# Optimization experiments

Measured on AMD Instinct MI355X. Metric: run time of the kernel, lower is better.

Reference implementation:

```python
import jax, jax.numpy as jnp
import numpy as np
import math

B, P, N, D = 64, 96, 12, 2048
W = P - N + 1  # 85 sliding windows
SCALE = 1.0 / math.sqrt(2048.0)
LN_EPS = 1e-5


def setup_inputs() -> dict:
    key = jax.random.key(0)
    ks = jax.random.split(key, 16)
    g = lambda k, shape: (jax.random.normal(k, shape, dtype=jnp.float32) * 0.02)
    return {
        "fc_feats": jax.random.normal(ks[0], (B, P, D), dtype=jnp.float32),
        "nsa_q_w": g(ks[1], (D, D)), "nsa_q_b": jnp.zeros((D,), jnp.float32),
        "nsa_k_w": g(ks[2], (D, D)), "nsa_k_b": jnp.zeros((D,), jnp.float32),
        "nsa_v_w": g(ks[3], (D, D)), "nsa_v_b": jnp.zeros((D,), jnp.float32),
        "nsa_fc_w": g(ks[4], (N, N)), "nsa_fc_b": jnp.zeros((N,), jnp.float32),
        "ds_w": g(ks[5], (W, P)), "ds_b": jnp.zeros((W,), jnp.float32),
        "ln_g": jnp.ones((D,), jnp.float32), "ln_b": jnp.zeros((D,), jnp.float32),
        "sa_q_w": g(ks[6], (D, D)), "sa_q_b": jnp.zeros((D,), jnp.float32),
        "sa_k_w": g(ks[7], (D, D)), "sa_k_b": jnp.zeros((D,), jnp.float32),
        "sa_v_w": g(ks[8], (D, D)), "sa_v_b": jnp.zeros((D,), jnp.float32),
        "sa_fc_w": g(ks[9], (W, W)), "sa_fc_b": jnp.zeros((W,), jnp.float32),
    }


def _encoder(fc_feats, nsa_q_w, nsa_q_b, nsa_k_w, nsa_k_b, nsa_v_w, nsa_v_b,
             nsa_fc_w, nsa_fc_b, ds_w, ds_b, ln_g, ln_b,
             sa_q_w, sa_q_b, sa_k_w, sa_k_b, sa_v_w, sa_v_b, sa_fc_w, sa_fc_b):
    # ---- Neighboring self-attention over all W sliding windows at once ----
    idx = jnp.arange(W)[:, None] + jnp.arange(N)[None, :]      # [W, N]
    win = fc_feats[:, idx, :]                                  # [B, W, N, D]
    q = jnp.einsum('bwnd,ed->bwne', win, nsa_q_w) + nsa_q_b
    k = jnp.einsum('bwnd,ed->bwne', win, nsa_k_w) + nsa_k_b
    v = jnp.einsum('bwnd,ed->bwne', win, nsa_v_w) + nsa_v_b
    attn = jax.nn.softmax(jnp.einsum('bwne,bwme->bwnm', q, k) * SCALE, axis=-1)
    nf = jnp.einsum('bwnm,bwmd->bwnd', attn, v)                # [B, W, N, D]
    # mask is a constant ones buffer [B,1,N] fed through fc + softmax
    mask = jnp.ones((B, N), jnp.float32)
    wmask = jax.nn.softmax(mask @ nsa_fc_w.T + nsa_fc_b, axis=-1)  # [B, N]
    nsa_feats = jnp.einsum('bn,bwnd->bwd', wmask, nf)          # [B, W, D]

    # ---- downsample over the image axis: Linear(P -> W) ----
    new_fc = jnp.einsum('bpd,wp->bwd', fc_feats, ds_w) + ds_b[None, :, None]

    # ---- residual + LayerNorm over D ----
    x = new_fc + nsa_feats
    mu = jnp.mean(x, axis=-1, keepdims=True)
    var = jnp.mean(jnp.square(x - mu), axis=-1, keepdims=True)
    x = (x - mu) * jax.lax.rsqrt(var + LN_EPS) * ln_g + ln_b   # [B, W, D]

    # ---- global self-attention over the W positions ----
    q2 = jnp.einsum('bwd,ed->bwe', x, sa_q_w) + sa_q_b
    k2 = jnp.einsum('bwd,ed->bwe', x, sa_k_w) + sa_k_b
    v2 = jnp.einsum('bwd,ed->bwe', x, sa_v_w) + sa_v_b
    attn2 = jax.nn.softmax(jnp.einsum('bwe,bue->bwu', q2, k2) * SCALE, axis=-1)
    nf2 = jnp.einsum('bwu,bud->bwd', attn2, v2)                # [B, W, D]
    mask2 = jnp.ones((B, W), jnp.float32)
    wmask2 = jax.nn.softmax(mask2 @ sa_fc_w.T + sa_fc_b, axis=-1)  # [B, W]
    return jnp.einsum('bw,bwd->bd', wmask2, nf2)               # [B, D]


def reference(fc_feats, nsa_q_w, nsa_q_b, nsa_k_w, nsa_k_b, nsa_v_w, nsa_v_b,
              nsa_fc_w, nsa_fc_b, ds_w, ds_b, ln_g, ln_b,
              sa_q_w, sa_q_b, sa_k_w, sa_k_b, sa_v_w, sa_v_b, sa_fc_w, sa_fc_b):
    return _encoder(fc_feats, nsa_q_w, nsa_q_b, nsa_k_w, nsa_k_b, nsa_v_w, nsa_v_b,
                    nsa_fc_w, nsa_fc_b, ds_w, ds_b, ln_g, ln_b,
                    sa_q_w, sa_q_b, sa_k_w, sa_k_b, sa_v_w, sa_v_b, sa_fc_w, sa_fc_b)
```

## Files before the change

kernel.cpp:

```cpp
#include <hip/hip_runtime.h>
#include <hip/hip_bf16.h>

#define DEV __device__ __forceinline__

typedef __attribute__((ext_vector_type(8))) short s16x8;
typedef __attribute__((ext_vector_type(4))) float f32x4;

#define B_ 64
#define P_ 96
#define N_ 12
#define D_ 2048
#define W_ 85
#define M1_ (B_ * P_)
#define M2_ (B_ * W_)
#define M2P_ 5504
#define SCALE_F 0.02209708691207961f
#define LN_EPS_F 1e-5f

DEV float b2f(short h) { return __uint_as_float(((unsigned)(unsigned short)h) << 16); }
DEV short f2b(float f) {
  __hip_bfloat16 h = __float2bfloat16(f);
  return *reinterpret_cast<short*>(&h);
}

DEV void gload_lds16(const void* g, void* l) {
  __builtin_amdgcn_global_load_lds(
      (const __attribute__((address_space(1))) unsigned int*)(unsigned long long)g,
      (__attribute__((address_space(3))) unsigned int*)(unsigned int)(unsigned long long)l,
      16, 0, 0);
}

__global__ __launch_bounds__(256) void castA_kernel(const float* s, short* d, int n) {
  const int i = (blockIdx.x * 256 + threadIdx.x) * 8;
  if (i >= n) return;
  float4 a = *(const float4*)(s + i);
  float4 b = *(const float4*)(s + i + 4);
  s16x8 o;
  o[0] = f2b(a.x); o[1] = f2b(a.y); o[2] = f2b(a.z); o[3] = f2b(a.w);
  o[4] = f2b(b.x); o[5] = f2b(b.y); o[6] = f2b(b.z); o[7] = f2b(b.w);
  *(s16x8*)(d + i) = o;
}

struct Cast2 { const float* s[2]; short* d[2]; };

__global__ __launch_bounds__(256) void cast2_kernel(Cast2 j, int n) {
  const int jb = blockIdx.y;
  const int i = (blockIdx.x * 256 + threadIdx.x) * 8;
  if (i >= n) return;
  const float* src = j.s[jb] + i;
  float4 a = *(const float4*)(src);
  float4 b = *(const float4*)(src + 4);
  s16x8 o;
  o[0] = f2b(a.x); o[1] = f2b(a.y); o[2] = f2b(a.z); o[3] = f2b(a.w);
  o[4] = f2b(b.x); o[5] = f2b(b.y); o[6] = f2b(b.z); o[7] = f2b(b.w);
  *(s16x8*)(j.d[jb] + i) = o;
}

struct Cast4T { const float* s[4]; short* d[4]; };

__global__ __launch_bounds__(256) void castT_kernel(Cast4T j) {
  __shared__ float tl[64][65];
  const int z = blockIdx.z;
  const float* src = j.s[z];
  short* dst = j.d[z];
  const int e0 = blockIdx.x * 64, d0 = blockIdx.y * 64;
  const int t = threadIdx.x;
  for (int i = t; i < 64 * 16; i += 256) {
    const int er = i >> 4, c4 = (i & 15) * 4;
    const float4 v = *(const float4*)(src + (long)(e0 + er) * 2048 + d0 + c4);
    tl[c4 + 0][er] = v.x;
    tl[c4 + 1][er] = v.y;
    tl[c4 + 2][er] = v.z;
    tl[c4 + 3][er] = v.w;
  }
  __syncthreads();
  for (int i = t; i < 64 * 8; i += 256) {
    const int dr = i >> 3, e8 = (i & 7) * 8;
    s16x8 o;
#pragma unroll
    for (int e = 0; e < 8; ++e) o[e] = f2b(tl[dr][e8 + e]);
    *(s16x8*)(dst + (long)(d0 + dr) * 2048 + e0 + e8) = o;
  }
}

__global__ __launch_bounds__(256) void prep_kernel(const float* nw, const float* nb,
                                                   const float* sw, const float* sb, float* wm,
                                                   const float* wk1, const float* bq1, float* r1,
                                                   const float* wk2, const float* bq2, float* r2) {
  const int bx = blockIdx.x, t = threadIdx.x;
  if (bx == 0) {
    __shared__ float l1[12], l2[85];
    if (t < 12) { float s = nb[t]; for (int n = 0; n < 12; ++n) s += nw[t * 12 + n]; l1[t] = s; }
    if (t < 85) { float s = sb[t]; for (int w = 0; w < 85; ++w) s += sw[t * 85 + w]; l2[t] = s; }
    __syncthreads();
    if (t == 0) {
      float m = l1[0]; for (int i = 1; i < 12; ++i) m = fmaxf(m, l1[i]);
      float s = 0.f; float e[12];
      for (int i = 0; i < 12; ++i) { e[i] = expf(l1[i] - m); s += e[i]; }
      for (int i = 0; i < 12; ++i) wm[i] = e[i] / s;
    } else if (t == 64) {
      float m = l2[0]; for (int i = 1; i < 85; ++i) m = fmaxf(m, l2[i]);
      float s = 0.f;
      for (int i = 0; i < 85; ++i) s += expf(l2[i] - m);
      for (int i = 0; i < 85; ++i) wm[16 + i] = expf(l2[i] - m) / s;
    }
    return;
  }
  const int idx = bx - 1;
  const int stage = idx >> 6;
  const int ec = (idx & 63) >> 3, dpc = idx & 7;
  const float* wk = stage ? wk2 : wk1;
  const float* bq = stage ? bq2 : bq1;
  float* r = stage ? r2 : r1;
  const int dp = dpc * 256 + t;
  const int e0 = ec * 256;
  float s = 0.f;
  for (int e = e0; e < e0 + 256; ++e) s += bq[e] * wk[(long)e * 2048 + dp];
  atomicAdd(&r[dp], s);
}

struct GemmArgs {
  const short* A[3];
  const short* Wt[3];
  const float* bias[3];
  void* C[3];
  int mlim;
};

template <int OM>
__global__ __launch_bounds__(256) void gemm_nt_bf16(GemmArgs g) {
  __shared__ short As[4096];
  __shared__ short Bs[4096];
  const int z = blockIdx.z;
  const short* A = g.A[z];
  const short* Wm = g.Wt[z];
  const int tid = threadIdx.x, wave = tid >> 6, lane = tid & 63;
  const int wmo = (wave >> 1) * 64, wno = (wave & 1) * 64;
  const long rowA0 = (long)blockIdx.x * 128;
  const long rowB0 = (long)blockIdx.y * 128;
  const int kg = lane >> 4, rsub = lane & 15;

  f32x4 acc[4][4];
  const f32x4 zz = {0.f, 0.f, 0.f, 0.f};
#pragma unroll
  for (int i = 0; i < 4; ++i)
#pragma unroll
    for (int jj = 0; jj < 4; ++jj) acc[i][jj] = zz;

  for (int kt = 0; kt < 64; ++kt) {
    const int kbase = kt * 32;
    __syncthreads();
#pragma unroll
    for (int i = 0; i < 2; ++i) {
      const int row = i * 64 + lane;
      gload_lds16(A + (rowA0 + row) * 2048 + kbase + wave * 8,
                  (char*)As + (wave * 128 + i * 64) * 16);
      gload_lds16(Wm + (rowB0 + row) * 2048 + kbase + wave * 8,
                  (char*)Bs + (wave * 128 + i * 64) * 16);
    }
    __syncthreads();
    s16x8 af[4], bv[4];
#pragma unroll
    for (int f = 0; f < 4; ++f) {
      af[f] = *(const s16x8*)(As + (kg * 128 + wmo + f * 16 + rsub) * 8);
      bv[f] = *(const s16x8*)(Bs + (kg * 128 + wno + f * 16 + rsub) * 8);
    }
#pragma unroll
    for (int i = 0; i < 4; ++i)
#pragma unroll
      for (int jj = 0; jj < 4; ++jj)
        acc[i][jj] = __builtin_amdgcn_mfma_f32_16x16x32_bf16(af[i], bv[jj], acc[i][jj], 0, 0, 0);
  }

  const float* bias = g.bias[z];
#pragma unroll
  for (int i = 0; i < 4; ++i) {
    const long row = rowA0 + wmo + i * 16 + (lane >> 4) * 4;
#pragma unroll
    for (int jj = 0; jj < 4; ++jj) {
      const long col = rowB0 + wno + jj * 16 + (lane & 15);
      const float bvl = bias ? bias[col] : 0.f;
#pragma unroll
      for (int r = 0; r < 4; ++r) {
        if (row + r < g.mlim) {
          if (OM == 0)
            ((short*)g.C[z])[(row + r) * 2048 + col] = f2b(acc[i][jj][r] + bvl);
          else
            ((float*)g.C[z])[(row + r) * 2048 + col] = acc[i][jj][r] + bvl;
        }
      }
    }
  }
}

template <int STAGE>
__global__ __launch_bounds__(256) void attn_mfma_kernel(const short* Aq, const short* Bk,
                                                        const float* wm, float* outp) {
  __shared__ short As[8][96][8];
  __shared__ short Bs[8][96][8];
  __shared__ float S[96][97];
  __shared__ float C1[85][12];
  __shared__ float M1[85][12];
  const int b = blockIdx.x;
  const int tid = threadIdx.x, wave = tid >> 6, lane = tid & 63;
  const int RPB = (STAGE == 1) ? 96 : 85;
  const long base = (long)b * RPB * 2048;
  const int wr0 = (wave >> 1) * 48, wc0 = (wave & 1) * 48;
  const int fr = lane & 15, fk = lane >> 4;

  f32x4 acc[3][3];
  const f32x4 zz = {0.f, 0.f, 0.f, 0.f};
#pragma unroll
  for (int i = 0; i < 3; ++i)
#pragma unroll
    for (int j = 0; j < 3; ++j) acc[i][j] = zz;

  for (int kt = 0; kt < 32; ++kt) {
    const int kb = kt * 64;
    __syncthreads();
#pragma unroll
    for (int it = 0; it < 3; ++it) {
      const int u = it * 256 + tid;
      const int row = u % 96, kg = u / 96;
      gload_lds16(Aq + base + (long)row * 2048 + kb + kg * 8, (char*)As + u * 16);
      gload_lds16(Bk + base + (long)row * 2048 + kb + kg * 8, (char*)Bs + u * 16);
    }
    __syncthreads();
#pragma unroll
    for (int ks = 0; ks < 2; ++ks) {
      const int kgx = ks * 4 + fk;
      s16x8 af[3], bv[3];
#pragma unroll
      for (int i = 0; i < 3; ++i) {
        af[i] = *(const s16x8*)&As[kgx][wr0 + i * 16 + fr][0];
        bv[i] = *(const s16x8*)&Bs[kgx][wc0 + i * 16 + fr][0];
      }
#pragma unroll
      for (int i = 0; i < 3; ++i)
#pragma unroll
        for (int j = 0; j < 3; ++j)
          acc[i][j] = __builtin_amdgcn_mfma_f32_16x16x32_bf16(af[i], bv[j], acc[i][j], 0, 0, 0);
    }
  }
#pragma unroll
  for (int i = 0; i < 3; ++i)
#pragma unroll
    for (int j = 0; j < 3; ++j)
#pragma unroll
      for (int r = 0; r < 4; ++r)
        S[wr0 + i * 16 + fk * 4 + r][wc0 + j * 16 + fr] = acc[i][j][r];
  __syncthreads();

  if (STAGE == 2) {
    if (tid < 85) {
      float mx = -1e30f;
      for (int u = 0; u < 85; ++u) mx = fmaxf(mx, S[tid][u]);
      float sum = 0.f;
      for (int u = 0; u < 85; ++u) {
        const float e = expf((S[tid][u] - mx) * SCALE_F);
        S[tid][u] = e;
        sum += e;
      }
      (&C1[0][0])[tid] = wm[tid] / sum;
    }
    __syncthreads();
    if (tid < 85) {
      float a = 0.f;
      for (int i = 0; i < 85; ++i) a += (&C1[0][0])[i] * S[i][tid];
      outp[b * 85 + tid] = a;
    }
  } else {
    for (int p = tid; p < 85 * 12; p += 256) {
      const int w = p / 12, n = p % 12;
      const int row = w + n;
      float mx = -1e30f;
      for (int m = 0; m < 12; ++m) mx = fmaxf(mx, S[row][w + m]);
      float sum = 0.f;
      for (int m = 0; m < 12; ++m) sum += expf((S[row][w + m] - mx) * SCALE_F);
      M1[w][n] = mx;
      C1[w][n] = wm[n] / sum;
    }
    __syncthreads();
    for (int p = tid; p < 85 * 12; p += 256) {
      const int w = p / 12, m = p % 12;
      float a = 0.f;
#pragma unroll
      for (int n = 0; n < 12; ++n)
        a += C1[w][n] * expf((S[w + n][w + m] - M1[w][n]) * SCALE_F);
      outp[(b * 85 + w) * 12 + m] = a;
    }
  }
}

__global__ __launch_bounds__(256) void combine_kernel(const float* fc32, const short* vp,
                                                      const float* p1, const float* dsw_g,
                                                      const float* dsb, float* X) {
  const int b = blockIdx.y, d0 = blockIdx.x * 128;
  const int t = threadIdx.x;
  __shared__ float fcs[96][128];
  __shared__ short vps[96][128];
  __shared__ float dsw[85][96];
  __shared__ float p1s[85][12];
  for (int s = t; s < 96 * 32; s += 256) {
    const int row = s >> 5, c4 = (s & 31) * 4;
    *(float4*)&fcs[row][c4] = *(const float4*)(fc32 + ((long)b * 96 + row) * 2048 + d0 + c4);
  }
  for (int s = t; s < 96 * 16; s += 256) {
    const int row = s >> 4, c8 = (s & 15) * 8;
    *(s16x8*)&vps[row][c8] = *(const s16x8*)(vp + ((long)b * 96 + row) * 2048 + d0 + c8);
  }
  for (int s = t; s < 85 * 96; s += 256) (&dsw[0][0])[s] = dsw_g[s];
  for (int s = t; s < 85 * 12; s += 256) (&p1s[0][0])[s] = p1[(long)b * 85 * 12 + s];
  __syncthreads();
  const int dp = (t & 63) * 2, wslot = t >> 6;
  for (int w = wslot; w < 85; w += 4) {
    float a0 = dsb[w], a1 = a0;
    for (int p = 0; p < 96; ++p) {
      const float c = dsw[w][p];
      a0 += c * fcs[p][dp];
      a1 += c * fcs[p][dp + 1];
    }
#pragma unroll
    for (int m = 0; m < 12; ++m) {
      const unsigned vv = *(const unsigned*)&vps[w + m][dp];
      const float c = p1s[w][m];
      a0 += c * __uint_as_float(vv << 16);
      a1 += c * __uint_as_float(vv & 0xffff0000u);
    }
    const long o = ((long)b * 85 + w) * 2048 + d0 + dp;
    X[o] = a0;
    X[o + 1] = a1;
  }
}

__global__ __launch_bounds__(256) void ln_kernel(const float* X, const float* gam,
                                                 const float* bet, short* XLN) {
  const long row = blockIdx.x;
  const int t = threadIdx.x;
  float v[8];
  *(float4*)&v[0] = *(const float4*)(X + row * 2048 + t * 8);
  *(float4*)&v[4] = *(const float4*)(X + row * 2048 + t * 8 + 4);
  float s = 0.f, q = 0.f;
#pragma unroll
  for (int e = 0; e < 8; ++e) { s += v[e]; q += v[e] * v[e]; }
#pragma unroll
  for (int o = 32; o > 0; o >>= 1) { s += __shfl_down(s, o); q += __shfl_down(q, o); }
  __shared__ float rs[4], rq[4];
  if ((t & 63) == 0) { rs[t >> 6] = s; rq[t >> 6] = q; }
  __syncthreads();
  const float S = rs[0] + rs[1] + rs[2] + rs[3];
  const float Q = rq[0] + rq[1] + rq[2] + rq[3];
  const float mu = S * (1.f / 2048.f);
  const float var = Q * (1.f / 2048.f) - mu * mu;
  const float rstd = rsqrtf(var + LN_EPS_F);
  s16x8 o8;
#pragma unroll
  for (int e = 0; e < 8; ++e) {
    const int c = t * 8 + e;
    o8[e] = f2b((v[e] - mu) * rstd * gam[c] + bet[c]);
  }
  *(s16x8*)(XLN + row * 2048 + t * 8) = o8;
}

__global__ __launch_bounds__(256) void z2_kernel(const short* xln, const float* p2, short* z2) {
  const int b = blockIdx.y, d = blockIdx.x * 256 + threadIdx.x;
  if (b >= 64) { z2[(long)b * 2048 + d] = 0; return; }
  __shared__ float pc[85];
  if (threadIdx.x < 85) pc[threadIdx.x] = p2[b * 85 + threadIdx.x];
  __syncthreads();
  float a = 0.f;
  for (int u = 0; u < 85; ++u) a += pc[u] * b2f(xln[((long)b * 85 + u) * 2048 + d]);
  z2[(long)b * 2048 + d] = f2b(a);
}

extern "C" void kernel_launch(void* const* d_in, const int* in_sizes, int n_in,
                              void* d_out, int out_size, void* d_ws, size_t ws_size,
                              hipStream_t stream) {
  char* ws = (char*)d_ws;
  size_t off = 0;
  auto alloc = [&](size_t bytes) -> char* {
    char* p = ws + off;
    off += (bytes + 255) & ~(size_t)255;
    return p;
  };

  short* A1   = (short*)alloc((size_t)M1_ * D_ * 2);
  short* WqT1 = (short*)alloc((size_t)D_ * D_ * 2);
  short* WkT1 = (short*)alloc((size_t)D_ * D_ * 2);
  short* WqT2 = (short*)alloc((size_t)D_ * D_ * 2);
  short* WkT2 = (short*)alloc((size_t)D_ * D_ * 2);
  short* Gt1  = (short*)alloc((size_t)D_ * D_ * 2);
  short* Gt2  = (short*)alloc((size_t)D_ * D_ * 2);
  short* Wv1c = (short*)alloc((size_t)D_ * D_ * 2);
  short* Wv2c = (short*)alloc((size_t)D_ * D_ * 2);
  short* Y1   = (short*)alloc((size_t)M1_ * D_ * 2);
  short* VP   = (short*)alloc((size_t)M1_ * D_ * 2);
  float* X    = (float*)alloc((size_t)M2_ * D_ * 4);
  float* P1   = (float*)alloc((size_t)B_ * W_ * N_ * 4);
  short* Z2   = (short*)alloc((size_t)128 * D_ * 2);
  float* P2   = (float*)alloc((size_t)B_ * W_ * 4);
  float* WM   = (float*)alloc(512);
  float* R1   = (float*)alloc(D_ * 4);
  float* R2   = (float*)alloc(D_ * 4);

  short* XLN = A1;
  short* Y2  = Y1;

  if (off > ws_size) return;

  const size_t zbytes = (size_t)((char*)R2 - (char*)P2) + D_ * 4;
  hipMemsetAsync(P2, 0, zbytes, stream);

  castA_kernel<<<dim3(6144), 256, 0, stream>>>((const float*)d_in[0], A1, M1_ * D_);
  Cast4T ct;
  ct.s[0] = (const float*)d_in[1];  ct.d[0] = WqT1;
  ct.s[1] = (const float*)d_in[3];  ct.d[1] = WkT1;
  ct.s[2] = (const float*)d_in[13]; ct.d[2] = WqT2;
  ct.s[3] = (const float*)d_in[15]; ct.d[3] = WkT2;
  castT_kernel<<<dim3(32, 32, 4), 256, 0, stream>>>(ct);
  Cast2 cv;
  cv.s[0] = (const float*)d_in[5];  cv.d[0] = Wv1c;
  cv.s[1] = (const float*)d_in[17]; cv.d[1] = Wv2c;
  cast2_kernel<<<dim3(2048, 2), 256, 0, stream>>>(cv, D_ * D_);
  prep_kernel<<<dim3(129), 256, 0, stream>>>(
      (const float*)d_in[7], (const float*)d_in[8],
      (const float*)d_in[19], (const float*)d_in[20], WM,
      (const float*)d_in[3], (const float*)d_in[2], R1,
      (const float*)d_in[15], (const float*)d_in[14], R2);

  GemmArgs gg;
  gg.A[0] = WkT1; gg.Wt[0] = WqT1; gg.bias[0] = nullptr; gg.C[0] = Gt1;
  gg.A[1] = WkT2; gg.Wt[1] = WqT2; gg.bias[1] = nullptr; gg.C[1] = Gt2;
  gg.mlim = 2048;
  gemm_nt_bf16<0><<<dim3(16, 16, 2), 256, 0, stream>>>(gg);

  GemmArgs g1;
  g1.A[0] = A1; g1.Wt[0] = Wv1c; g1.bias[0] = (const float*)d_in[6]; g1.C[0] = VP;
  g1.A[1] = A1; g1.Wt[1] = Gt1;  g1.bias[1] = R1;                    g1.C[1] = Y1;
  g1.mlim = M1_;
  gemm_nt_bf16<0><<<dim3(48, 16, 2), 256, 0, stream>>>(g1);

  attn_mfma_kernel<1><<<dim3(64), 256, 0, stream>>>(Y1, A1, WM, P1);

  combine_kernel<<<dim3(16, 64), 256, 0, stream>>>((const float*)d_in[0], VP, P1,
                                                   (const float*)d_in[9],
                                                   (const float*)d_in[10], X);
  ln_kernel<<<dim3(5440), 256, 0, stream>>>(X, (const float*)d_in[11], (const float*)d_in[12], XLN);

  GemmArgs g2;
  g2.A[0] = XLN; g2.Wt[0] = Gt2; g2.bias[0] = R2; g2.C[0] = Y2;
  g2.mlim = M2P_;
  gemm_nt_bf16<0><<<dim3(43, 16, 1), 256, 0, stream>>>(g2);

  attn_mfma_kernel<2><<<dim3(64), 256, 0, stream>>>(Y2, XLN, WM + 16, P2);

  z2_kernel<<<dim3(8, 128), 256, 0, stream>>>(XLN, P2, Z2);

  GemmArgs go;
  go.A[0] = Z2; go.Wt[0] = Wv2c; go.bias[0] = (const float*)d_in[18]; go.C[0] = d_out;
  go.mlim = 64;
  gemm_nt_bf16<1><<<dim3(1, 16, 1), 256, 0, stream>>>(go);
}
```

Before: 889.9 us.

## Double-buffer LDS tiles in GEMM/attention and split-K the output GEMM

Adds LDS double buffering to the main bf16 GEMM and the attention score kernels, so the global-to-LDS load of the next K tile overlaps the MFMA work on the current one and one barrier per iteration is dropped. Replaces the single-block-row output GEMM (16 blocks) with a dedicated split-K kernel using 64 blocks that accumulates into the output with atomics, after a memset of the output. It also shrinks the Z2 padding from 128 to 64 rows. The cost is doubled LDS use, which may lower occupancy, plus float atomics and their nondeterministic summation order.

```diff
diff --git a/kernel.cpp b/kernel.cpp
--- a/kernel.cpp
+++ b/kernel.cpp
@@ -129,8 +129,8 @@
 
 template <int OM>
 __global__ __launch_bounds__(256) void gemm_nt_bf16(GemmArgs g) {
-  __shared__ short As[4096];
-  __shared__ short Bs[4096];
+  __shared__ short As[2][4096];
+  __shared__ short Bs[2][4096];
   const int z = blockIdx.z;
   const short* A = g.A[z];
   const short* Wm = g.Wt[z];
@@ -147,29 +147,34 @@
 #pragma unroll
     for (int jj = 0; jj < 4; ++jj) acc[i][jj] = zz;
 
-  for (int kt = 0; kt < 64; ++kt) {
-    const int kbase = kt * 32;
-    __syncthreads();
+  auto stage = [&](int bb, int kbase) {
 #pragma unroll
     for (int i = 0; i < 2; ++i) {
       const int row = i * 64 + lane;
       gload_lds16(A + (rowA0 + row) * 2048 + kbase + wave * 8,
-                  (char*)As + (wave * 128 + i * 64) * 16);
+                  (char*)As[bb] + (wave * 128 + i * 64) * 16);
       gload_lds16(Wm + (rowB0 + row) * 2048 + kbase + wave * 8,
-                  (char*)Bs + (wave * 128 + i * 64) * 16);
-    }
-    __syncthreads();
+                  (char*)Bs[bb] + (wave * 128 + i * 64) * 16);
+    }
+  };
+
+  stage(0, 0);
+  __syncthreads();
+  for (int kt = 0; kt < 64; ++kt) {
+    const int cur = kt & 1;
+    if (kt < 63) stage(cur ^ 1, (kt + 1) * 32);
     s16x8 af[4], bv[4];
 #pragma unroll
     for (int f = 0; f < 4; ++f) {
-      af[f] = *(const s16x8*)(As + (kg * 128 + wmo + f * 16 + rsub) * 8);
-      bv[f] = *(const s16x8*)(Bs + (kg * 128 + wno + f * 16 + rsub) * 8);
+      af[f] = *(const s16x8*)(As[cur] + (kg * 128 + wmo + f * 16 + rsub) * 8);
+      bv[f] = *(const s16x8*)(Bs[cur] + (kg * 128 + wno + f * 16 + rsub) * 8);
     }
 #pragma unroll
     for (int i = 0; i < 4; ++i)
 #pragma unroll
       for (int jj = 0; jj < 4; ++jj)
         acc[i][jj] = __builtin_amdgcn_mfma_f32_16x16x32_bf16(af[i], bv[jj], acc[i][jj], 0, 0, 0);
+    __syncthreads();
   }
 
   const float* bias = g.bias[z];
@@ -193,11 +198,69 @@
   }
 }
 
+__global__ __launch_bounds__(256) void out_gemm_kernel(const short* A, const short* Wm,
+                                                       const float* bias, float* C) {
+  __shared__ short As[2][4][64][8];
+  __shared__ short Bs[2][4][128][8];
+  const int kz = blockIdx.x;
+  const long rowB0 = (long)blockIdx.y * 128;
+  const int tid = threadIdx.x, wave = tid >> 6, lane = tid & 63;
+  const int wno = wave * 32;
+  const int kgx = lane >> 4, rsub = lane & 15;
+
+  f32x4 acc[4][2];
+  const f32x4 zz = {0.f, 0.f, 0.f, 0.f};
+#pragma unroll
+  for (int f = 0; f < 4; ++f) { acc[f][0] = zz; acc[f][1] = zz; }
+
+  auto stage = [&](int bb, int kbase) {
+    gload_lds16(A + (long)lane * 2048 + kbase + wave * 8, (char*)As[bb] + tid * 16);
+#pragma unroll
+    for (int i = 0; i < 2; ++i) {
+      const int row = i * 64 + lane;
+      gload_lds16(Wm + (rowB0 + row) * 2048 + kbase + wave * 8,
+                  (char*)Bs[bb] + (wave * 128 + i * 64) * 16);
+    }
+  };
+
+  const int kb0 = kz * 512;
+  stage(0, kb0);
+  __syncthreads();
+  for (int kt = 0; kt < 16; ++kt) {
+    const int cur = kt & 1;
+    if (kt < 15) stage(cur ^ 1, kb0 + (kt + 1) * 32);
+    s16x8 af[4], bv[2];
+#pragma unroll
+    for (int f = 0; f < 4; ++f) af[f] = *(const s16x8*)&As[cur][kgx][f * 16 + rsub][0];
+#pragma unroll
+    for (int j = 0; j < 2; ++j) bv[j] = *(const s16x8*)&Bs[cur][kgx][wno + j * 16 + rsub][0];
+#pragma unroll
+    for (int f = 0; f < 4; ++f)
+#pragma unroll
+      for (int j = 0; j < 2; ++j)
+        acc[f][j] = __builtin_amdgcn_mfma_f32_16x16x32_bf16(af[f], bv[j], acc[f][j], 0, 0, 0);
+    __syncthreads();
+  }
+
+#pragma unroll
+  for (int f = 0; f < 4; ++f) {
+    const int row = f * 16 + (lane >> 4) * 4;
+#pragma unroll
+    for (int j = 0; j < 2; ++j) {
+      const long col = rowB0 + wno + j * 16 + (lane & 15);
+      const float bvl = (kz == 0) ? bias[col] : 0.f;
+#pragma unroll
+      for (int r = 0; r < 4; ++r)
+        atomicAdd(&C[(long)(row + r) * 2048 + col], acc[f][j][r] + bvl);
+    }
+  }
+}
+
 template <int STAGE>
 __global__ __launch_bounds__(256) void attn_mfma_kernel(const short* Aq, const short* Bk,
                                                         const float* wm, float* outp) {
-  __shared__ short As[8][96][8];
-  __shared__ short Bs[8][96][8];
+  __shared__ short As[2][8][96][8];
+  __shared__ short Bs[2][8][96][8];
   __shared__ float S[96][97];
   __shared__ float C1[85][12];
   __shared__ float M1[85][12];
@@ -215,25 +278,29 @@
 #pragma unroll
     for (int j = 0; j < 3; ++j) acc[i][j] = zz;
 
-  for (int kt = 0; kt < 32; ++kt) {
-    const int kb = kt * 64;
-    __syncthreads();
+  auto stage = [&](int bb, int kb) {
 #pragma unroll
     for (int it = 0; it < 3; ++it) {
       const int u = it * 256 + tid;
       const int row = u % 96, kg = u / 96;
-      gload_lds16(Aq + base + (long)row * 2048 + kb + kg * 8, (char*)As + u * 16);
-      gload_lds16(Bk + base + (long)row * 2048 + kb + kg * 8, (char*)Bs + u * 16);
-    }
-    __syncthreads();
+      gload_lds16(Aq + base + (long)row * 2048 + kb + kg * 8, (char*)As[bb] + u * 16);
+      gload_lds16(Bk + base + (long)row * 2048 + kb + kg * 8, (char*)Bs[bb] + u * 16);
+    }
+  };
+
+  stage(0, 0);
+  __syncthreads();
+  for (int kt = 0; kt < 32; ++kt) {
+    const int cur = kt & 1;
+    if (kt < 31) stage(cur ^ 1, (kt + 1) * 64);
 #pragma unroll
     for (int ks = 0; ks < 2; ++ks) {
       const int kgx = ks * 4 + fk;
       s16x8 af[3], bv[3];
 #pragma unroll
       for (int i = 0; i < 3; ++i) {
-        af[i] = *(const s16x8*)&As[kgx][wr0 + i * 16 + fr][0];
-        bv[i] = *(const s16x8*)&Bs[kgx][wc0 + i * 16 + fr][0];
+        af[i] = *(const s16x8*)&As[cur][kgx][wr0 + i * 16 + fr][0];
+        bv[i] = *(const s16x8*)&Bs[cur][kgx][wc0 + i * 16 + fr][0];
       }
 #pragma unroll
       for (int i = 0; i < 3; ++i)
@@ -241,6 +308,7 @@
         for (int j = 0; j < 3; ++j)
           acc[i][j] = __builtin_amdgcn_mfma_f32_16x16x32_bf16(af[i], bv[j], acc[i][j], 0, 0, 0);
     }
+    __syncthreads();
   }
 #pragma unroll
   for (int i = 0; i < 3; ++i)
@@ -364,7 +432,6 @@
 
 __global__ __launch_bounds__(256) void z2_kernel(const short* xln, const float* p2, short* z2) {
   const int b = blockIdx.y, d = blockIdx.x * 256 + threadIdx.x;
-  if (b >= 64) { z2[(long)b * 2048 + d] = 0; return; }
   __shared__ float pc[85];
   if (threadIdx.x < 85) pc[threadIdx.x] = p2[b * 85 + threadIdx.x];
   __syncthreads();
@@ -397,7 +464,7 @@
   short* VP   = (short*)alloc((size_t)M1_ * D_ * 2);
   float* X    = (float*)alloc((size_t)M2_ * D_ * 4);
   float* P1   = (float*)alloc((size_t)B_ * W_ * N_ * 4);
-  short* Z2   = (short*)alloc((size_t)128 * D_ * 2);
+  short* Z2   = (short*)alloc((size_t)64 * D_ * 2);
   float* P2   = (float*)alloc((size_t)B_ * W_ * 4);
   float* WM   = (float*)alloc(512);
   float* R1   = (float*)alloc(D_ * 4);
@@ -410,6 +477,7 @@
 
   const size_t zbytes = (size_t)((char*)R2 - (char*)P2) + D_ * 4;
   hipMemsetAsync(P2, 0, zbytes, stream);
+  hipMemsetAsync(d_out, 0, (size_t)B_ * D_ * 4, stream);
 
   castA_kernel<<<dim3(6144), 256, 0, stream>>>((const float*)d_in[0], A1, M1_ * D_);
   Cast4T ct;
@@ -454,10 +522,8 @@
 
   attn_mfma_kernel<2><<<dim3(64), 256, 0, stream>>>(Y2, XLN, WM + 16, P2);
 
-  z2_kernel<<<dim3(8, 128), 256, 0, stream>>>(XLN, P2, Z2);
-
-  GemmArgs go;
-  go.A[0] = Z2; go.Wt[0] = Wv2c; go.bias[0] = (const float*)d_in[18]; go.C[0] = d_out;
-  go.mlim = 64;
-  gemm_nt_bf16<1><<<dim3(1, 16, 1), 256, 0, stream>>>(go);
-}
+  z2_kernel<<<dim3(8, 64), 256, 0, stream>>>(XLN, P2, Z2);
+
+  out_gemm_kernel<<<dim3(4, 16), 256, 0, stream>>>(Z2, Wv2c, (const float*)d_in[18],
+                                                   (float*)d_out);
+}
```

After: 841.7 us. 5.4% less time.
